# Performance work log

Measured on AMD Instinct MI355X. Metric: run time of the kernel, lower is better.

Reference implementation:

```python
import jax, jax.numpy as jnp
import numpy as np
import math

B, T, S, C, W = 32, 512, 128, 30, 10  # batch, seq, spans, candidates, max span width
D_CTX, D_ENT, H, V = 768, 300, 100, 200000
EPS = 1e-5
NEG = -1e30


def layer_norm(x, g, b):
    mu = jnp.mean(x, axis=-1, keepdims=True)
    var = jnp.mean((x - mu) ** 2, axis=-1, keepdims=True)
    return (x - mu) / jnp.sqrt(var + EPS) * g + b


def setup_inputs() -> dict:
    key = jax.random.key(0)
    ks = jax.random.split(key, 12)
    contextual_embeddings = jax.random.normal(ks[0], (B, T, D_CTX), jnp.float32)
    mask = jnp.ones((B, T), jnp.int32)
    starts = jax.random.randint(ks[1], (B, S), 0, T - W)
    widths = jax.random.randint(ks[2], (B, S), 0, W)
    ends = starts + widths  # inclusive end, AllenNLP convention
    # pad last 8 spans per example with -1 to exercise span masking
    pad = jnp.arange(S)[None, :] >= S - 8
    starts = jnp.where(pad, -1, starts)
    ends = jnp.where(pad, -1, ends)
    candidate_spans = jnp.stack([starts, ends], axis=-1)
    candidate_entities = jax.random.randint(ks[3], (B, S, C), 1, V)
    pri = jax.random.uniform(ks[4], (B, S, C), jnp.float32)
    candidate_entity_priors = pri / pri.sum(-1, keepdims=True)
    candidate_segment_ids = jnp.zeros((B, S, C), jnp.int32)
    # parameters
    entity_table = jax.random.normal(ks[5], (V, D_ENT), jnp.float32) * 0.02
    proj_W = jax.random.normal(ks[6], (D_ENT, D_CTX), jnp.float32) * 0.02
    proj_b = jnp.zeros((D_ENT,), jnp.float32)
    kg_g = jnp.ones((D_ENT,), jnp.float32)
    kg_b = jnp.zeros((D_ENT,), jnp.float32)
    ln_g = jnp.ones((D_ENT,), jnp.float32)
    ln_b = jnp.zeros((D_ENT,), jnp.float32)
    attn_W = jax.random.normal(ks[7], (1, D_ENT), jnp.float32) * 0.02
    attn_b = jnp.zeros((1,), jnp.float32)
    W1 = jax.random.normal(ks[8], (H, 2), jnp.float32) * 0.02
    b1 = jnp.zeros((H,), jnp.float32)
    W2 = jax.random.normal(ks[9], (1, H), jnp.float32) * 0.02
    b2 = jnp.zeros((1,), jnp.float32)
    return dict(contextual_embeddings=contextual_embeddings, mask=mask,
                candidate_spans=candidate_spans, candidate_entities=candidate_entities,
                candidate_entity_priors=candidate_entity_priors,
                candidate_segment_ids=candidate_segment_ids,
                entity_table=entity_table, proj_W=proj_W, proj_b=proj_b,
                kg_g=kg_g, kg_b=kg_b, ln_g=ln_g, ln_b=ln_b,
                attn_W=attn_W, attn_b=attn_b, W1=W1, b1=b1, W2=W2, b2=b2)


def reference(contextual_embeddings, mask, candidate_spans, candidate_entities,
              candidate_entity_priors, candidate_segment_ids, entity_table,
              proj_W, proj_b, kg_g, kg_b, ln_g, ln_b, attn_W, attn_b,
              W1, b1, W2, b2):
    # --- entity embedding lookup + KG layer norm ---
    ent_emb = layer_norm(entity_table[candidate_entities], kg_g, kg_b)  # (B,S,C,D)

    # --- bert -> kg projection ---
    proj = contextual_embeddings @ proj_W.T + proj_b  # (B,T,D_ENT)

    span_mask = candidate_spans[:, :, 0] > -1  # (B,S)

    # --- SelfAttentiveSpanExtractor ---
    att_logits = (proj @ attn_W.T + attn_b)[..., 0]  # (B,T)
    starts = candidate_spans[..., 0]
    ends = candidate_spans[..., 1]
    widths = ends - starts
    offs = jnp.arange(W)  # max span width
    idx = starts[..., None] + offs  # (B,S,W)
    valid = (offs <= widths[..., None]) & (idx >= 0) & (idx < T)
    idx_c = jnp.where(valid, idx, 0)
    idx_flat = idx_c.reshape(B, S * W)
    span_emb = jnp.take_along_axis(proj, idx_flat[..., None], axis=1).reshape(B, S, W, D_ENT)
    span_log = jnp.take_along_axis(att_logits, idx_flat, axis=1).reshape(B, S, W)
    attn = jax.nn.softmax(jnp.where(valid, span_log, NEG), axis=-1)  # (B,S,W)
    span_rep = jnp.einsum('bsw,bswd->bsd', attn, span_emb)
    span_rep = span_rep * span_mask[..., None].astype(span_rep.dtype)
    span_rep = layer_norm(span_rep, ln_g, ln_b)  # (B,S,D)

    # --- DotAttentionWithPrior ---
    scores = jnp.einsum('bsd,bscd->bsc', span_rep, ent_emb) / math.sqrt(D_ENT)
    feat = jnp.stack([scores, candidate_entity_priors], axis=-1)  # (B,S,C,2)
    h = jax.nn.relu(feat @ W1.T + b1)
    link = (h @ W2.T + b2)[..., 0]  # (B,S,C)
    entity_mask = candidate_entities > 0
    linking_scores = jnp.where(entity_mask, link, -10000.0)
    normed = jax.nn.softmax(linking_scores, axis=-1)
    weighted = jnp.einsum('bsc,bscd->bsd', normed, ent_emb)
    return linking_scores, weighted
```

## Files before the change

### kernel.cpp

```cpp
#include <hip/hip_runtime.h>
#include <hip/hip_bf16.h>
#include <math.h>

#define BB 32
#define TT 512
#define SS 128
#define CC 30
#define WW 10
#define DCTX 768
#define DENT 300
#define HH 100
#define EPSF 1e-5f
#define NEGF -1e30f

typedef __attribute__((ext_vector_type(8))) short bf16x8;
typedef __attribute__((ext_vector_type(4))) float f32x4;

#define NK  (DCTX / 32)
#define NCT 20

__device__ __forceinline__ float wave_sum(float v) {
    #pragma unroll
    for (int off = 32; off > 0; off >>= 1) v += __shfl_xor(v, off);
    return v;
}

__device__ __forceinline__ ushort f2bf(float f) {
    __hip_bfloat16 h = __float2bfloat16(f);
    return *reinterpret_cast<ushort*>(&h);
}

__device__ __forceinline__ float dot4(float4 a, float4 b) {
    return a.x*b.x + a.y*b.y + a.z*b.z + a.w*b.w;
}
__device__ __forceinline__ float hadd8(float4 a, float4 b) {
    return a.x+a.y+a.z+a.w + b.x+b.y+b.z+b.w;
}
__device__ __forceinline__ ushort4 cvt4(float4 v) {
    ushort4 h; h.x = f2bf(v.x); h.y = f2bf(v.y); h.z = f2bf(v.z); h.w = f2bf(v.w);
    return h;
}

__global__ __launch_bounds__(256) void wpre_kernel(
    const float* __restrict__ Wt, ushort* __restrict__ wpre)
{
    const int g = blockIdx.x * 256 + threadIdx.x;
    const int l = g & 63;
    const int t = (g >> 6) % NK;
    const int ct = g / (NK * 64);
    const int col = ct * 16 + (l & 15);
    const int k = t * 32 + (l >> 4) * 8;
    ushort4 h0 = {0, 0, 0, 0}, h1 = {0, 0, 0, 0};
    if (col < DENT) {
        float4 v0 = *(const float4*)(Wt + (size_t)col * DCTX + k);
        float4 v1 = *(const float4*)(Wt + (size_t)col * DCTX + k + 4);
        h0 = cvt4(v0); h1 = cvt4(v1);
    }
    *(ushort4*)(wpre + (size_t)g * 8)     = h0;
    *(ushort4*)(wpre + (size_t)g * 8 + 4) = h1;
}

#define GBM 64
#define LDA 40

__global__ __launch_bounds__(512) void gemm_proj_mfma(
    const float*  __restrict__ A,
    const ushort* __restrict__ wpre,
    const float*  __restrict__ bias,
    float* __restrict__ out)
{
    __shared__ ushort Al[2][GBM * LDA];
    const int tid = threadIdx.x;
    const int lane = tid & 63;
    const int wv = tid >> 6;
    const int wm = wv >> 2;
    const int wn = wv & 3;
    const int m0 = blockIdx.x * GBM;
    const int ar = tid >> 3;
    const int ak = (tid & 7) * 4;
    const int lr = lane & 15;
    const int kq = (lane >> 4) * 8;

    const float* aP = A + (size_t)(m0 + ar) * DCTX + ak;
    const ushort* bp = wpre + (size_t)wn * 5 * NK * 512 + (size_t)lane * 8;

    f32x4 acc[2][5];
    #pragma unroll
    for (int i = 0; i < 2; ++i)
        #pragma unroll
        for (int j = 0; j < 5; ++j)
            acc[i][j] = (f32x4){0.f, 0.f, 0.f, 0.f};

    bf16x8 cb[5], nb[5];
    #pragma unroll
    for (int j = 0; j < 5; ++j)
        cb[j] = *(const bf16x8*)(bp + (size_t)j * NK * 512);

#define STOREA(BUF, v_) (*(ushort4*)&Al[BUF][ar * LDA + ak] = cvt4(v_))

#define COMPUTE(BUF) do {                                                      \
        bf16x8 af_[2];                                                         \
        _Pragma("unroll")                                                      \
        for (int i_ = 0; i_ < 2; ++i_)                                         \
            af_[i_] = *(const bf16x8*)&Al[BUF][(wm*32 + i_*16 + lr)*LDA + kq]; \
        _Pragma("unroll")                                                      \
        for (int j_ = 0; j_ < 5; ++j_)                                         \
            acc[0][j_] = __builtin_amdgcn_mfma_f32_16x16x32_bf16(              \
                af_[0], cb[j_], acc[0][j_], 0, 0, 0);                          \
        _Pragma("unroll")                                                      \
        for (int j_ = 0; j_ < 5; ++j_)                                         \
            acc[1][j_] = __builtin_amdgcn_mfma_f32_16x16x32_bf16(              \
                af_[1], cb[j_], acc[1][j_], 0, 0, 0);                          \
    } while (0)

    float4 avA = *(const float4*)(aP);
    float4 avB = *(const float4*)(aP + 32);
    STOREA(0, avA);
    __syncthreads();

    #pragma unroll 1
    for (int kk = 0; kk < NK; kk += 2) {
        #pragma unroll
        for (int j = 0; j < 5; ++j)
            nb[j] = *(const bf16x8*)(bp + ((size_t)j * NK + kk + 1) * 512);
        if (kk + 2 < NK) avA = *(const float4*)(aP + (kk + 2) * 32);
        COMPUTE(0);
        STOREA(1, avB);
        __syncthreads();
        #pragma unroll
        for (int j = 0; j < 5; ++j) cb[j] = nb[j];
        if (kk + 2 < NK) {
            #pragma unroll
            for (int j = 0; j < 5; ++j)
                nb[j] = *(const bf16x8*)(bp + ((size_t)j * NK + kk + 2) * 512);
            avB = *(const float4*)(aP + (kk + 3) * 32);
        }
        COMPUTE(1);
        if (kk + 2 < NK) STOREA(0, avA);
        __syncthreads();
        #pragma unroll
        for (int j = 0; j < 5; ++j) cb[j] = nb[j];
    }

    const int lq = lane >> 4;
    #pragma unroll
    for (int j = 0; j < 5; ++j) {
        int col = wn * 80 + j * 16 + lr;
        if (col < DENT) {
            float bv = bias[col];
            #pragma unroll
            for (int i = 0; i < 2; ++i)
                #pragma unroll
                for (int r = 0; r < 4; ++r) {
                    int row = m0 + wm * 32 + i * 16 + lq * 4 + r;
                    out[(size_t)row * DENT + col] = acc[i][j][r] + bv;
                }
        }
    }
}

__global__ __launch_bounds__(256) void span_kernel(
    const float* __restrict__ proj,
    const int*   __restrict__ spans,
    const float* __restrict__ attn_W,
    const float* __restrict__ attn_b,
    const float* __restrict__ ln_g,
    const float* __restrict__ ln_b,
    const float* __restrict__ kg_g,
    const float* __restrict__ kg_b,
    float* __restrict__ srg_out,
    float* __restrict__ sgsb)
{
    const int bs = blockIdx.x * 4 + (threadIdx.x >> 6);
    const int b = bs >> 7;
    const int lane = threadIdx.x & 63;
    const int start = spans[bs * 2 + 0];
    const int end   = spans[bs * 2 + 1];
    const int width = end - start;
    const bool lo = lane < 11;
    const float4 z = make_float4(0.f, 0.f, 0.f, 0.f);

    const float4* attW4 = (const float4*)attn_W;
    float4 w0 = attW4[lane];
    float4 w1 = lo ? attW4[64 + lane] : z;

    float4 a0[WW], a1[WW];
    float slog[WW];
    bool vld[WW];
    #pragma unroll
    for (int w = 0; w < WW; ++w) {
        int idx = start + w;
        vld[w] = (w <= width) && (idx >= 0) && (idx < TT);
        const float4* pr = (const float4*)(proj + (size_t)(b * TT + (vld[w] ? idx : 0)) * DENT);
        a0[w] = pr[lane];
        a1[w] = lo ? pr[64 + lane] : z;
        slog[w] = dot4(a0[w], w0) + dot4(a1[w], w1);
    }
    const float ab = attn_b[0];
    #pragma unroll
    for (int w = 0; w < WW; ++w) {
        float r = wave_sum(slog[w]);
        slog[w] = vld[w] ? r + ab : NEGF;
    }
    float m = slog[0];
    #pragma unroll
    for (int w = 1; w < WW; ++w) m = fmaxf(m, slog[w]);
    float den = 0.f;
    float aw[WW];
    #pragma unroll
    for (int w = 0; w < WW; ++w) { aw[w] = expf(slog[w] - m); den += aw[w]; }
    const float inv = 1.f / den;
    const float msk = (start > -1) ? inv : 0.f;

    float4 acc0 = z, acc1 = z;
    #pragma unroll
    for (int w = 0; w < WW; ++w) {
        float c = aw[w] * msk;
        acc0.x = fmaf(c, a0[w].x, acc0.x); acc0.y = fmaf(c, a0[w].y, acc0.y);
        acc0.z = fmaf(c, a0[w].z, acc0.z); acc0.w = fmaf(c, a0[w].w, acc0.w);
        acc1.x = fmaf(c, a1[w].x, acc1.x); acc1.y = fmaf(c, a1[w].y, acc1.y);
        acc1.z = fmaf(c, a1[w].z, acc1.z); acc1.w = fmaf(c, a1[w].w, acc1.w);
    }
    float s1 = hadd8(acc0, acc1);
    float s2 = dot4(acc0, acc0) + dot4(acc1, acc1);
    #pragma unroll
    for (int off = 32; off > 0; off >>= 1) {
        s1 += __shfl_xor(s1, off);
        s2 += __shfl_xor(s2, off);
    }
    const float mu = s1 * (1.f / DENT);
    const float rstd = rsqrtf(s2 * (1.f / DENT) - mu * mu + EPSF);

    const float4* lg4 = (const float4*)ln_g;  const float4* lb4 = (const float4*)ln_b;
    const float4* gg4 = (const float4*)kg_g;  const float4* gb4 = (const float4*)kg_b;
    float pg = 0.f, pb = 0.f;
    float4* so = (float4*)(srg_out + (size_t)bs * DENT);
    {
        float4 g = lg4[lane], bb_ = lb4[lane], gg = gg4[lane], gb = gb4[lane];
        float4 val;
        val.x = fmaf((acc0.x - mu) * rstd, g.x, bb_.x);
        val.y = fmaf((acc0.y - mu) * rstd, g.y, bb_.y);
        val.z = fmaf((acc0.z - mu) * rstd, g.z, bb_.z);
        val.w = fmaf((acc0.w - mu) * rstd, g.w, bb_.w);
        float4 vg = make_float4(val.x * gg.x, val.y * gg.y, val.z * gg.z, val.w * gg.w);
        so[lane] = vg;
        pg += vg.x + vg.y + vg.z + vg.w;
        pb += val.x * gb.x + val.y * gb.y + val.z * gb.z + val.w * gb.w;
    }
    if (lo) {
        float4 g = lg4[64 + lane], bb_ = lb4[64 + lane], gg = gg4[64 + lane], gb = gb4[64 + lane];
        float4 val;
        val.x = fmaf((acc1.x - mu) * rstd, g.x, bb_.x);
        val.y = fmaf((acc1.y - mu) * rstd, g.y, bb_.y);
        val.z = fmaf((acc1.z - mu) * rstd, g.z, bb_.z);
        val.w = fmaf((acc1.w - mu) * rstd, g.w, bb_.w);
        float4 vg = make_float4(val.x * gg.x, val.y * gg.y, val.z * gg.z, val.w * gg.w);
        so[64 + lane] = vg;
        pg += vg.x + vg.y + vg.z + vg.w;
        pb += val.x * gb.x + val.y * gb.y + val.z * gb.z + val.w * gb.w;
    }
    #pragma unroll
    for (int off = 32; off > 0; off >>= 1) {
        pg += __shfl_xor(pg, off);
        pb += __shfl_xor(pb, off);
    }
    if (lane == 0) { sgsb[bs * 2 + 0] = pg; sgsb[bs * 2 + 1] = pb; }
}

__global__ __launch_bounds__(512) void final_fused(
    const float* __restrict__ srg,
    const float* __restrict__ sgsb,
    const int*   __restrict__ cand,
    const float* __restrict__ priors,
    const float* __restrict__ table,
    const float* __restrict__ W1,
    const float* __restrict__ b1,
    const float* __restrict__ W2,
    const float* __restrict__ b2,
    const float* __restrict__ kg_g,
    const float* __restrict__ kg_b,
    float* __restrict__ out_link,
    float* __restrict__ out_w)
{
    __shared__ float rows[CC][DENT];
    __shared__ float smu[CC], srs[CC], ssc[CC], sexp[CC];
    const int bs = blockIdx.x;
    const int tid = threadIdx.x;
    const int lane = tid & 63;
    const int wv = tid >> 6;
    const bool lo = lane < 11;
    const float4 z = make_float4(0.f, 0.f, 0.f, 0.f);

    const int c0 = wv, c1 = wv + 8, c2 = wv + 16, c3 = wv + 24;
    const bool has3 = (c3 < CC);
    const int e0 = cand[bs * CC + c0];
    const int e1 = cand[bs * CC + c1];
    const int e2 = cand[bs * CC + c2];
    const int e3 = has3 ? cand[bs * CC + c3] : e2;

    const float4* r0 = (const float4*)(table + (size_t)e0 * DENT);
    const float4* r1 = (const float4*)(table + (size_t)e1 * DENT);
    const float4* r2 = (const float4*)(table + (size_t)e2 * DENT);
    const float4* r3 = (const float4*)(table + (size_t)e3 * DENT);
    float4 xa0 = r0[lane], xa1 = r1[lane], xa2 = r2[lane], xa3 = r3[lane];
    float4 xb0 = lo ? r0[64 + lane] : z;
    float4 xb1 = lo ? r1[64 + lane] : z;
    float4 xb2 = lo ? r2[64 + lane] : z;
    float4 xb3 = lo ? r3[64 + lane] : z;

    const float4* sg4 = (const float4*)(srg + (size_t)bs * DENT);
    float4 g0 = sg4[lane];
    float4 g1 = lo ? sg4[64 + lane] : z;
    const float SG = sgsb[bs * 2 + 0];
    const float SB = sgsb[bs * 2 + 1];

    const float W1a0 = W1[2 * lane], W1b0 = W1[2 * lane + 1];
    const float B10 = b1[lane], W20 = W2[lane];
    float W1a1 = 0.f, W1b1 = 0.f, B11 = 0.f, W21 = 0.f;
    if (lane < HH - 64) {
        int j = lane + 64;
        W1a1 = W1[2 * j]; W1b1 = W1[2 * j + 1]; B11 = b1[j]; W21 = W2[j];
    }
    const float b2v = b2[0];
    const float p0 = priors[bs * CC + c0];
    const float p1 = priors[bs * CC + c1];
    const float p2 = priors[bs * CC + c2];
    const float p3 = has3 ? priors[bs * CC + c3] : 0.f;

    *(float4*)&rows[c0][lane * 4] = xa0;
    *(float4*)&rows[c1][lane * 4] = xa1;
    *(float4*)&rows[c2][lane * 4] = xa2;
    if (has3) *(float4*)&rows[c3][lane * 4] = xa3;
    if (lo) {
        *(float4*)&rows[c0][256 + lane * 4] = xb0;
        *(float4*)&rows[c1][256 + lane * 4] = xb1;
        *(float4*)&rows[c2][256 + lane * 4] = xb2;
        if (has3) *(float4*)&rows[c3][256 + lane * 4] = xb3;
    }

    float s1_0 = hadd8(xa0, xb0), s1_1 = hadd8(xa1, xb1);
    float s1_2 = hadd8(xa2, xb2), s1_3 = hadd8(xa3, xb3);
    float s2_0 = dot4(xa0, xa0) + dot4(xb0, xb0), s2_1 = dot4(xa1, xa1) + dot4(xb1, xb1);
    float s2_2 = dot4(xa2, xa2) + dot4(xb2, xb2), s2_3 = dot4(xa3, xa3) + dot4(xb3, xb3);
    float s3_0 = dot4(g0, xa0) + dot4(g1, xb0), s3_1 = dot4(g0, xa1) + dot4(g1, xb1);
    float s3_2 = dot4(g0, xa2) + dot4(g1, xb2), s3_3 = dot4(g0, xa3) + dot4(g1, xb3);
    #pragma unroll
    for (int off = 32; off > 0; off >>= 1) {
        s1_0 += __shfl_xor(s1_0, off); s1_1 += __shfl_xor(s1_1, off);
        s1_2 += __shfl_xor(s1_2, off); s1_3 += __shfl_xor(s1_3, off);
        s2_0 += __shfl_xor(s2_0, off); s2_1 += __shfl_xor(s2_1, off);
        s2_2 += __shfl_xor(s2_2, off); s2_3 += __shfl_xor(s2_3, off);
        s3_0 += __shfl_xor(s3_0, off); s3_1 += __shfl_xor(s3_1, off);
        s3_2 += __shfl_xor(s3_2, off); s3_3 += __shfl_xor(s3_3, off);
    }
    const float isd = rsqrtf((float)DENT);

#define CAND_TAIL(K, CK, EK, PK)                                               \
    do {                                                                       \
        float mu_ = s1_##K * (1.f / DENT);                                     \
        float rstd_ = rsqrtf(s2_##K * (1.f / DENT) - mu_ * mu_ + EPSF);        \
        float score_ = (rstd_ * (s3_##K - mu_ * SG) + SB) * isd;               \
        float h_ = fmaxf(fmaf(W1a0, score_, fmaf(W1b0, PK, B10)), 0.f);        \
        float h2_ = fmaxf(fmaf(W1a1, score_, fmaf(W1b1, PK, B11)), 0.f);       \
        float lp_ = fmaf(W21, h2_, W20 * h_);                                  \
        lp_ = wave_sum(lp_) + b2v;                                             \
        float link_ = (EK > 0) ? lp_ : -10000.0f;                              \
        if (lane == 0) {                                                       \
            smu[CK] = mu_; srs[CK] = rstd_; ssc[CK] = link_;                   \
            out_link[bs * CC + CK] = link_;                                    \
        }                                                                      \
    } while (0)

    CAND_TAIL(0, c0, e0, p0);
    CAND_TAIL(1, c1, e1, p1);
    CAND_TAIL(2, c2, e2, p2);
    if (has3) CAND_TAIL(3, c3, e3, p3);
    __syncthreads();

    if (tid < CC) {
        float m = ssc[0];
        #pragma unroll
        for (int c = 1; c < CC; ++c) m = fmaxf(m, ssc[c]);
        sexp[tid] = expf(ssc[tid] - m);
    }
    __syncthreads();

    const int d = tid;
    if (d < DENT) {
        float den = 0.f;
        #pragma unroll
        for (int c = 0; c < CC; ++c) den += sexp[c];
        const float inv = 1.f / den;
        float acc = 0.f, S2 = 0.f, sn = 0.f;
        #pragma unroll
        for (int c = 0; c < CC; ++c) {
            float n = sexp[c] * inv;
            float coef = n * srs[c];
            acc = fmaf(coef, rows[c][d], acc);
            S2 = fmaf(coef, smu[c], S2);
            sn += n;
        }
        out_w[(size_t)bs * DENT + d] = kg_g[d] * (acc - S2) + kg_b[d] * sn;
    }
}

extern "C" void kernel_launch(void* const* d_in, const int* in_sizes, int n_in,
                              void* d_out, int out_size, void* d_ws, size_t ws_size,
                              hipStream_t stream) {
    const float* ctx    = (const float*)d_in[0];
    const int*   spans  = (const int*)d_in[2];
    const int*   cand   = (const int*)d_in[3];
    const float* priors = (const float*)d_in[4];
    const float* table  = (const float*)d_in[6];
    const float* projW  = (const float*)d_in[7];
    const float* projb  = (const float*)d_in[8];
    const float* kg_g   = (const float*)d_in[9];
    const float* kg_b   = (const float*)d_in[10];
    const float* ln_g   = (const float*)d_in[11];
    const float* ln_b   = (const float*)d_in[12];
    const float* attW   = (const float*)d_in[13];
    const float* attb   = (const float*)d_in[14];
    const float* W1     = (const float*)d_in[15];
    const float* b1     = (const float*)d_in[16];
    const float* W2     = (const float*)d_in[17];
    const float* b2     = (const float*)d_in[18];

    float* proj = (float*)d_ws;
    float* srg  = proj + (size_t)BB * TT * DENT;
    float* sgsb = srg + (size_t)BB * SS * DENT;
    ushort* wpre = (ushort*)srg;

    float* out_link = (float*)d_out;
    float* out_w    = out_link + (size_t)BB * SS * CC;

    wpre_kernel<<<NCT * NK * 64 / 256, 256, 0, stream>>>(projW, wpre);
    gemm_proj_mfma<<<BB * TT / GBM, 512, 0, stream>>>(ctx, wpre, projb, proj);
    span_kernel<<<BB * SS / 4, 256, 0, stream>>>(proj, spans, attW, attb,
                                                 ln_g, ln_b, kg_g, kg_b, srg, sgsb);
    final_fused<<<BB * SS, 512, 0, stream>>>(srg, sgsb, cand, priors, table,
                                             W1, b1, W2, b2, kg_g, kg_b,
                                             out_link, out_w);
}
```

Before: 95.21 us.

## Store projection as bf16 and fuse span pooling into final kernel

The projection GEMM now writes its output as bf16 with a padded row stride of 320 instead of fp32. The separate span kernel is removed, and its attention pooling, layer norm and kg-gain preparation run in wave 0 of the final fused kernel, with results passed through shared memory. This removes one launch, the srg/sgsb round trip through global memory, and halves projection traffic. In exchange it adds bf16 rounding on proj and places the span work serially on one wave before the other waves can compute scores.

```diff
diff --git a/kernel.cpp b/kernel.cpp
--- a/kernel.cpp
+++ b/kernel.cpp
@@ -12,6 +12,7 @@
 #define HH 100
 #define EPSF 1e-5f
 #define NEGF -1e30f
+#define PSTR 320
 
 typedef __attribute__((ext_vector_type(8))) short bf16x8;
 typedef __attribute__((ext_vector_type(4))) float f32x4;
@@ -28,6 +29,16 @@
 __device__ __forceinline__ ushort f2bf(float f) {
     __hip_bfloat16 h = __float2bfloat16(f);
     return *reinterpret_cast<ushort*>(&h);
+}
+
+__device__ __forceinline__ float bf2f1(short s) {
+    union { unsigned u; float f; } t;
+    t.u = ((unsigned)(unsigned short)s) << 16;
+    return t.f;
+}
+__device__ __forceinline__ void bf8_cvt(bf16x8 v, float4& lo, float4& hi) {
+    lo.x = bf2f1(v[0]); lo.y = bf2f1(v[1]); lo.z = bf2f1(v[2]); lo.w = bf2f1(v[3]);
+    hi.x = bf2f1(v[4]); hi.y = bf2f1(v[5]); hi.z = bf2f1(v[6]); hi.w = bf2f1(v[7]);
 }
 
 __device__ __forceinline__ float dot4(float4 a, float4 b) {
@@ -52,9 +63,8 @@
     const int k = t * 32 + (l >> 4) * 8;
     ushort4 h0 = {0, 0, 0, 0}, h1 = {0, 0, 0, 0};
     if (col < DENT) {
-        float4 v0 = *(const float4*)(Wt + (size_t)col * DCTX + k);
-        float4 v1 = *(const float4*)(Wt + (size_t)col * DCTX + k + 4);
-        h0 = cvt4(v0); h1 = cvt4(v1);
+        h0 = cvt4(*(const float4*)(Wt + (size_t)col * DCTX + k));
+        h1 = cvt4(*(const float4*)(Wt + (size_t)col * DCTX + k + 4));
     }
     *(ushort4*)(wpre + (size_t)g * 8)     = h0;
     *(ushort4*)(wpre + (size_t)g * 8 + 4) = h1;
@@ -67,7 +77,7 @@
     const float*  __restrict__ A,
     const ushort* __restrict__ wpre,
     const float*  __restrict__ bias,
-    float* __restrict__ out)
+    ushort* __restrict__ out)
 {
     __shared__ ushort Al[2][GBM * LDA];
     const int tid = threadIdx.x;
@@ -146,145 +156,42 @@
     #pragma unroll
     for (int j = 0; j < 5; ++j) {
         int col = wn * 80 + j * 16 + lr;
-        if (col < DENT) {
-            float bv = bias[col];
+        float bv = (col < DENT) ? bias[col] : 0.f;
+        #pragma unroll
+        for (int i = 0; i < 2; ++i)
             #pragma unroll
-            for (int i = 0; i < 2; ++i)
-                #pragma unroll
-                for (int r = 0; r < 4; ++r) {
-                    int row = m0 + wm * 32 + i * 16 + lq * 4 + r;
-                    out[(size_t)row * DENT + col] = acc[i][j][r] + bv;
-                }
-        }
-    }
-}
-
-__global__ __launch_bounds__(256) void span_kernel(
-    const float* __restrict__ proj,
-    const int*   __restrict__ spans,
-    const float* __restrict__ attn_W,
-    const float* __restrict__ attn_b,
-    const float* __restrict__ ln_g,
-    const float* __restrict__ ln_b,
-    const float* __restrict__ kg_g,
-    const float* __restrict__ kg_b,
-    float* __restrict__ srg_out,
-    float* __restrict__ sgsb)
-{
-    const int bs = blockIdx.x * 4 + (threadIdx.x >> 6);
-    const int b = bs >> 7;
-    const int lane = threadIdx.x & 63;
-    const int start = spans[bs * 2 + 0];
-    const int end   = spans[bs * 2 + 1];
-    const int width = end - start;
-    const bool lo = lane < 11;
-    const float4 z = make_float4(0.f, 0.f, 0.f, 0.f);
-
-    const float4* attW4 = (const float4*)attn_W;
-    float4 w0 = attW4[lane];
-    float4 w1 = lo ? attW4[64 + lane] : z;
-
-    float4 a0[WW], a1[WW];
-    float slog[WW];
-    bool vld[WW];
-    #pragma unroll
-    for (int w = 0; w < WW; ++w) {
-        int idx = start + w;
-        vld[w] = (w <= width) && (idx >= 0) && (idx < TT);
-        const float4* pr = (const float4*)(proj + (size_t)(b * TT + (vld[w] ? idx : 0)) * DENT);
-        a0[w] = pr[lane];
-        a1[w] = lo ? pr[64 + lane] : z;
-        slog[w] = dot4(a0[w], w0) + dot4(a1[w], w1);
-    }
-    const float ab = attn_b[0];
-    #pragma unroll
-    for (int w = 0; w < WW; ++w) {
-        float r = wave_sum(slog[w]);
-        slog[w] = vld[w] ? r + ab : NEGF;
-    }
-    float m = slog[0];
-    #pragma unroll
-    for (int w = 1; w < WW; ++w) m = fmaxf(m, slog[w]);
-    float den = 0.f;
-    float aw[WW];
-    #pragma unroll
-    for (int w = 0; w < WW; ++w) { aw[w] = expf(slog[w] - m); den += aw[w]; }
-    const float inv = 1.f / den;
-    const float msk = (start > -1) ? inv : 0.f;
-
-    float4 acc0 = z, acc1 = z;
-    #pragma unroll
-    for (int w = 0; w < WW; ++w) {
-        float c = aw[w] * msk;
-        acc0.x = fmaf(c, a0[w].x, acc0.x); acc0.y = fmaf(c, a0[w].y, acc0.y);
-        acc0.z = fmaf(c, a0[w].z, acc0.z); acc0.w = fmaf(c, a0[w].w, acc0.w);
-        acc1.x = fmaf(c, a1[w].x, acc1.x); acc1.y = fmaf(c, a1[w].y, acc1.y);
-        acc1.z = fmaf(c, a1[w].z, acc1.z); acc1.w = fmaf(c, a1[w].w, acc1.w);
-    }
-    float s1 = hadd8(acc0, acc1);
-    float s2 = dot4(acc0, acc0) + dot4(acc1, acc1);
-    #pragma unroll
-    for (int off = 32; off > 0; off >>= 1) {
-        s1 += __shfl_xor(s1, off);
-        s2 += __shfl_xor(s2, off);
-    }
-    const float mu = s1 * (1.f / DENT);
-    const float rstd = rsqrtf(s2 * (1.f / DENT) - mu * mu + EPSF);
-
-    const float4* lg4 = (const float4*)ln_g;  const float4* lb4 = (const float4*)ln_b;
-    const float4* gg4 = (const float4*)kg_g;  const float4* gb4 = (const float4*)kg_b;
-    float pg = 0.f, pb = 0.f;
-    float4* so = (float4*)(srg_out + (size_t)bs * DENT);
-    {
-        float4 g = lg4[lane], bb_ = lb4[lane], gg = gg4[lane], gb = gb4[lane];
-        float4 val;
-        val.x = fmaf((acc0.x - mu) * rstd, g.x, bb_.x);
-        val.y = fmaf((acc0.y - mu) * rstd, g.y, bb_.y);
-        val.z = fmaf((acc0.z - mu) * rstd, g.z, bb_.z);
-        val.w = fmaf((acc0.w - mu) * rstd, g.w, bb_.w);
-        float4 vg = make_float4(val.x * gg.x, val.y * gg.y, val.z * gg.z, val.w * gg.w);
-        so[lane] = vg;
-        pg += vg.x + vg.y + vg.z + vg.w;
-        pb += val.x * gb.x + val.y * gb.y + val.z * gb.z + val.w * gb.w;
-    }
-    if (lo) {
-        float4 g = lg4[64 + lane], bb_ = lb4[64 + lane], gg = gg4[64 + lane], gb = gb4[64 + lane];
-        float4 val;
-        val.x = fmaf((acc1.x - mu) * rstd, g.x, bb_.x);
-        val.y = fmaf((acc1.y - mu) * rstd, g.y, bb_.y);
-        val.z = fmaf((acc1.z - mu) * rstd, g.z, bb_.z);
-        val.w = fmaf((acc1.w - mu) * rstd, g.w, bb_.w);
-        float4 vg = make_float4(val.x * gg.x, val.y * gg.y, val.z * gg.z, val.w * gg.w);
-        so[64 + lane] = vg;
-        pg += vg.x + vg.y + vg.z + vg.w;
-        pb += val.x * gb.x + val.y * gb.y + val.z * gb.z + val.w * gb.w;
-    }
-    #pragma unroll
-    for (int off = 32; off > 0; off >>= 1) {
-        pg += __shfl_xor(pg, off);
-        pb += __shfl_xor(pb, off);
-    }
-    if (lane == 0) { sgsb[bs * 2 + 0] = pg; sgsb[bs * 2 + 1] = pb; }
+            for (int r = 0; r < 4; ++r) {
+                int row = m0 + wm * 32 + i * 16 + lq * 4 + r;
+                out[(size_t)row * PSTR + col] = f2bf(acc[i][j][r] + bv);
+            }
+    }
 }
 
 __global__ __launch_bounds__(512) void final_fused(
-    const float* __restrict__ srg,
-    const float* __restrict__ sgsb,
-    const int*   __restrict__ cand,
-    const float* __restrict__ priors,
-    const float* __restrict__ table,
-    const float* __restrict__ W1,
-    const float* __restrict__ b1,
-    const float* __restrict__ W2,
-    const float* __restrict__ b2,
-    const float* __restrict__ kg_g,
-    const float* __restrict__ kg_b,
+    const ushort* __restrict__ proj,
+    const int*    __restrict__ spans,
+    const float*  __restrict__ attW,
+    const float*  __restrict__ attb,
+    const float*  __restrict__ ln_g,
+    const float*  __restrict__ ln_b,
+    const float*  __restrict__ kg_g,
+    const float*  __restrict__ kg_b,
+    const int*    __restrict__ cand,
+    const float*  __restrict__ priors,
+    const float*  __restrict__ table,
+    const float*  __restrict__ W1,
+    const float*  __restrict__ b1,
+    const float*  __restrict__ W2,
+    const float*  __restrict__ b2,
     float* __restrict__ out_link,
     float* __restrict__ out_w)
 {
     __shared__ float rows[CC][DENT];
+    __shared__ float s_srg[PSTR];
     __shared__ float smu[CC], srs[CC], ssc[CC], sexp[CC];
+    __shared__ float sSG, sSB;
     const int bs = blockIdx.x;
+    const int b = bs >> 7;
     const int tid = threadIdx.x;
     const int lane = tid & 63;
     const int wv = tid >> 6;
@@ -308,25 +215,6 @@
     float4 xb2 = lo ? r2[64 + lane] : z;
     float4 xb3 = lo ? r3[64 + lane] : z;
 
-    const float4* sg4 = (const float4*)(srg + (size_t)bs * DENT);
-    float4 g0 = sg4[lane];
-    float4 g1 = lo ? sg4[64 + lane] : z;
-    const float SG = sgsb[bs * 2 + 0];
-    const float SB = sgsb[bs * 2 + 1];
-
-    const float W1a0 = W1[2 * lane], W1b0 = W1[2 * lane + 1];
-    const float B10 = b1[lane], W20 = W2[lane];
-    float W1a1 = 0.f, W1b1 = 0.f, B11 = 0.f, W21 = 0.f;
-    if (lane < HH - 64) {
-        int j = lane + 64;
-        W1a1 = W1[2 * j]; W1b1 = W1[2 * j + 1]; B11 = b1[j]; W21 = W2[j];
-    }
-    const float b2v = b2[0];
-    const float p0 = priors[bs * CC + c0];
-    const float p1 = priors[bs * CC + c1];
-    const float p2 = priors[bs * CC + c2];
-    const float p3 = has3 ? priors[bs * CC + c3] : 0.f;
-
     *(float4*)&rows[c0][lane * 4] = xa0;
     *(float4*)&rows[c1][lane * 4] = xa1;
     *(float4*)&rows[c2][lane * 4] = xa2;
@@ -342,17 +230,136 @@
     float s1_2 = hadd8(xa2, xb2), s1_3 = hadd8(xa3, xb3);
     float s2_0 = dot4(xa0, xa0) + dot4(xb0, xb0), s2_1 = dot4(xa1, xa1) + dot4(xb1, xb1);
     float s2_2 = dot4(xa2, xa2) + dot4(xb2, xb2), s2_3 = dot4(xa3, xa3) + dot4(xb3, xb3);
-    float s3_0 = dot4(g0, xa0) + dot4(g1, xb0), s3_1 = dot4(g0, xa1) + dot4(g1, xb1);
-    float s3_2 = dot4(g0, xa2) + dot4(g1, xb2), s3_3 = dot4(g0, xa3) + dot4(g1, xb3);
     #pragma unroll
     for (int off = 32; off > 0; off >>= 1) {
         s1_0 += __shfl_xor(s1_0, off); s1_1 += __shfl_xor(s1_1, off);
         s1_2 += __shfl_xor(s1_2, off); s1_3 += __shfl_xor(s1_3, off);
         s2_0 += __shfl_xor(s2_0, off); s2_1 += __shfl_xor(s2_1, off);
         s2_2 += __shfl_xor(s2_2, off); s2_3 += __shfl_xor(s2_3, off);
+    }
+
+    if (wv == 0) {
+        const int start = spans[bs * 2 + 0];
+        const int end   = spans[bs * 2 + 1];
+        const int width = end - start;
+        const bool L   = lane < 40;
+        const int  dl  = (L ? lane : 39) * 8;
+        const bool ga  = L && (dl < DENT);
+        const bool gb4 = L && (dl + 4 < DENT);
+
+        float4 w0v = ga  ? *(const float4*)(attW + dl)     : z;
+        float4 w1v = gb4 ? *(const float4*)(attW + dl + 4) : z;
+
+        float slog[WW];
+        int rbase[WW];
+        bool vld[WW];
+        #pragma unroll
+        for (int w = 0; w < WW; ++w) {
+            int idx = start + w;
+            vld[w] = (w <= width) && (idx >= 0) && (idx < TT);
+            rbase[w] = (b * TT + (vld[w] ? idx : 0)) * PSTR;
+            bf16x8 v = *(const bf16x8*)(proj + rbase[w] + dl);
+            float4 plo, phi; bf8_cvt(v, plo, phi);
+            if (!L) { plo = z; phi = z; }
+            slog[w] = dot4(plo, w0v) + dot4(phi, w1v);
+        }
+        const float ab = attb[0];
+        #pragma unroll
+        for (int w = 0; w < WW; ++w) {
+            float r = wave_sum(slog[w]);
+            slog[w] = vld[w] ? r + ab : NEGF;
+        }
+        float m = slog[0];
+        #pragma unroll
+        for (int w = 1; w < WW; ++w) m = fmaxf(m, slog[w]);
+        float den = 0.f;
+        float aw[WW];
+        #pragma unroll
+        for (int w = 0; w < WW; ++w) { aw[w] = expf(slog[w] - m); den += aw[w]; }
+        const float msk = (start > -1) ? (1.f / den) : 0.f;
+
+        float4 acc0 = z, acc1 = z;
+        #pragma unroll
+        for (int w = 0; w < WW; ++w) {
+            bf16x8 v = *(const bf16x8*)(proj + rbase[w] + dl);
+            float4 plo, phi; bf8_cvt(v, plo, phi);
+            if (!L) { plo = z; phi = z; }
+            float c = aw[w] * msk;
+            acc0.x = fmaf(c, plo.x, acc0.x); acc0.y = fmaf(c, plo.y, acc0.y);
+            acc0.z = fmaf(c, plo.z, acc0.z); acc0.w = fmaf(c, plo.w, acc0.w);
+            acc1.x = fmaf(c, phi.x, acc1.x); acc1.y = fmaf(c, phi.y, acc1.y);
+            acc1.z = fmaf(c, phi.z, acc1.z); acc1.w = fmaf(c, phi.w, acc1.w);
+        }
+        float s1 = hadd8(acc0, acc1);
+        float s2 = dot4(acc0, acc0) + dot4(acc1, acc1);
+        #pragma unroll
+        for (int off = 32; off > 0; off >>= 1) {
+            s1 += __shfl_xor(s1, off);
+            s2 += __shfl_xor(s2, off);
+        }
+        const float mu = s1 * (1.f / DENT);
+        const float rstd = rsqrtf(s2 * (1.f / DENT) - mu * mu + EPSF);
+
+        float4 lg0 = ga  ? *(const float4*)(ln_g + dl)     : z;
+        float4 lg1 = gb4 ? *(const float4*)(ln_g + dl + 4) : z;
+        float4 lb0 = ga  ? *(const float4*)(ln_b + dl)     : z;
+        float4 lb1 = gb4 ? *(const float4*)(ln_b + dl + 4) : z;
+        float4 gg0 = ga  ? *(const float4*)(kg_g + dl)     : z;
+        float4 gg1 = gb4 ? *(const float4*)(kg_g + dl + 4) : z;
+        float4 gbv0 = ga  ? *(const float4*)(kg_b + dl)     : z;
+        float4 gbv1 = gb4 ? *(const float4*)(kg_b + dl + 4) : z;
+
+        float4 val0, val1, vg0, vg1;
+        val0.x = fmaf((acc0.x - mu) * rstd, lg0.x, lb0.x);
+        val0.y = fmaf((acc0.y - mu) * rstd, lg0.y, lb0.y);
+        val0.z = fmaf((acc0.z - mu) * rstd, lg0.z, lb0.z);
+        val0.w = fmaf((acc0.w - mu) * rstd, lg0.w, lb0.w);
+        val1.x = fmaf((acc1.x - mu) * rstd, lg1.x, lb1.x);
+        val1.y = fmaf((acc1.y - mu) * rstd, lg1.y, lb1.y);
+        val1.z = fmaf((acc1.z - mu) * rstd, lg1.z, lb1.z);
+        val1.w = fmaf((acc1.w - mu) * rstd, lg1.w, lb1.w);
+        vg0 = make_float4(val0.x*gg0.x, val0.y*gg0.y, val0.z*gg0.z, val0.w*gg0.w);
+        vg1 = make_float4(val1.x*gg1.x, val1.y*gg1.y, val1.z*gg1.z, val1.w*gg1.w);
+        if (L) {
+            *(float4*)&s_srg[dl]     = vg0;
+            *(float4*)&s_srg[dl + 4] = vg1;
+        }
+        float pg = hadd8(vg0, vg1);
+        float pb = dot4(val0, gbv0) + dot4(val1, gbv1);
+        #pragma unroll
+        for (int off = 32; off > 0; off >>= 1) {
+            pg += __shfl_xor(pg, off);
+            pb += __shfl_xor(pb, off);
+        }
+        if (lane == 0) { sSG = pg; sSB = pb; }
+    }
+    __syncthreads();
+
+    const float4 g0 = *(const float4*)&s_srg[lane * 4];
+    const float4 g1 = lo ? *(const float4*)&s_srg[256 + lane * 4] : z;
+    const float SG = sSG;
+    const float SB = sSB;
+
+    float s3_0 = dot4(g0, xa0) + dot4(g1, xb0), s3_1 = dot4(g0, xa1) + dot4(g1, xb1);
+    float s3_2 = dot4(g0, xa2) + dot4(g1, xb2), s3_3 = dot4(g0, xa3) + dot4(g1, xb3);
+    #pragma unroll
+    for (int off = 32; off > 0; off >>= 1) {
         s3_0 += __shfl_xor(s3_0, off); s3_1 += __shfl_xor(s3_1, off);
         s3_2 += __shfl_xor(s3_2, off); s3_3 += __shfl_xor(s3_3, off);
     }
+
+    const float W1a0 = W1[2 * lane], W1b0 = W1[2 * lane + 1];
+    const float B10 = b1[lane], W20 = W2[lane];
+    float W1a1 = 0.f, W1b1 = 0.f, B11 = 0.f, W21 = 0.f;
+    if (lane < HH - 64) {
+        int j = lane + 64;
+        W1a1 = W1[2 * j]; W1b1 = W1[2 * j + 1]; B11 = b1[j]; W21 = W2[j];
+    }
+    const float b2v = b2[0];
+    const float p0 = priors[bs * CC + c0];
+    const float p1 = priors[bs * CC + c1];
+    const float p2 = priors[bs * CC + c2];
+    const float p3 = has3 ? priors[bs * CC + c3] : 0.f;
     const float isd = rsqrtf((float)DENT);
 
 #define CAND_TAIL(K, CK, EK, PK)                                               \
@@ -425,19 +432,17 @@
     const float* W2     = (const float*)d_in[17];
     const float* b2     = (const float*)d_in[18];
 
-    float* proj = (float*)d_ws;
-    float* srg  = proj + (size_t)BB * TT * DENT;
-    float* sgsb = srg + (size_t)BB * SS * DENT;
-    ushort* wpre = (ushort*)srg;
+    ushort* proj = (ushort*)d_ws;
+    ushort* wpre = proj + (size_t)BB * TT * PSTR;
 
     float* out_link = (float*)d_out;
     float* out_w    = out_link + (size_t)BB * SS * CC;
 
     wpre_kernel<<<NCT * NK * 64 / 256, 256, 0, stream>>>(projW, wpre);
     gemm_proj_mfma<<<BB * TT / GBM, 512, 0, stream>>>(ctx, wpre, projb, proj);
-    span_kernel<<<BB * SS / 4, 256, 0, stream>>>(proj, spans, attW, attb,
-                                                 ln_g, ln_b, kg_g, kg_b, srg, sgsb);
-    final_fused<<<BB * SS, 512, 0, stream>>>(srg, sgsb, cand, priors, table,
-                                             W1, b1, W2, b2, kg_g, kg_b,
+    final_fused<<<BB * SS, 512, 0, stream>>>(proj, spans, attW, attb,
+                                             ln_g, ln_b, kg_g, kg_b,
+                                             cand, priors, table,
+                                             W1, b1, W2, b2,
                                              out_link, out_w);
 }
```

New measurement: 212.3 us. 2.23x slower.

## Process two span rows per block in final kernel with early gathers

Applied to the files above, without the earlier changes.

The final fused kernel now handles two (batch, span) pairs per block, issuing the entity-table gathers for both up front so the second pair's loads overlap the first pair's reductions and softmax. The grid is halved. This aims to hide gather latency and amortise block overhead, at the cost of many more live registers (up to 16 extra float4 per thread), which may reduce occupancy, plus an extra barrier.

```diff
diff --git a/kernel.cpp b/kernel.cpp
--- a/kernel.cpp
+++ b/kernel.cpp
@@ -52,9 +52,8 @@
     const int k = t * 32 + (l >> 4) * 8;
     ushort4 h0 = {0, 0, 0, 0}, h1 = {0, 0, 0, 0};
     if (col < DENT) {
-        float4 v0 = *(const float4*)(Wt + (size_t)col * DCTX + k);
-        float4 v1 = *(const float4*)(Wt + (size_t)col * DCTX + k + 4);
-        h0 = cvt4(v0); h1 = cvt4(v1);
+        h0 = cvt4(*(const float4*)(Wt + (size_t)col * DCTX + k));
+        h1 = cvt4(*(const float4*)(Wt + (size_t)col * DCTX + k + 4));
     }
     *(ushort4*)(wpre + (size_t)g * 8)     = h0;
     *(ushort4*)(wpre + (size_t)g * 8 + 4) = h1;
@@ -283,8 +282,10 @@
     float* __restrict__ out_w)
 {
     __shared__ float rows[CC][DENT];
-    __shared__ float smu[CC], srs[CC], ssc[CC], sexp[CC];
-    const int bs = blockIdx.x;
+    __shared__ float smuA[CC], srsA[CC], sscA[CC], sexpA[CC];
+    __shared__ float smuB[CC], srsB[CC], sscB[CC], sexpB[CC];
+    const int bs0 = blockIdx.x * 2;
+    const int bs1 = bs0 + 1;
     const int tid = threadIdx.x;
     const int lane = tid & 63;
     const int wv = tid >> 6;
@@ -293,26 +294,40 @@
 
     const int c0 = wv, c1 = wv + 8, c2 = wv + 16, c3 = wv + 24;
     const bool has3 = (c3 < CC);
-    const int e0 = cand[bs * CC + c0];
-    const int e1 = cand[bs * CC + c1];
-    const int e2 = cand[bs * CC + c2];
-    const int e3 = has3 ? cand[bs * CC + c3] : e2;
-
-    const float4* r0 = (const float4*)(table + (size_t)e0 * DENT);
-    const float4* r1 = (const float4*)(table + (size_t)e1 * DENT);
-    const float4* r2 = (const float4*)(table + (size_t)e2 * DENT);
-    const float4* r3 = (const float4*)(table + (size_t)e3 * DENT);
-    float4 xa0 = r0[lane], xa1 = r1[lane], xa2 = r2[lane], xa3 = r3[lane];
-    float4 xb0 = lo ? r0[64 + lane] : z;
-    float4 xb1 = lo ? r1[64 + lane] : z;
-    float4 xb2 = lo ? r2[64 + lane] : z;
-    float4 xb3 = lo ? r3[64 + lane] : z;
-
-    const float4* sg4 = (const float4*)(srg + (size_t)bs * DENT);
-    float4 g0 = sg4[lane];
-    float4 g1 = lo ? sg4[64 + lane] : z;
-    const float SG = sgsb[bs * 2 + 0];
-    const float SB = sgsb[bs * 2 + 1];
+
+    const int e00 = cand[bs0 * CC + c0];
+    const int e01 = cand[bs0 * CC + c1];
+    const int e02 = cand[bs0 * CC + c2];
+    const int e03 = has3 ? cand[bs0 * CC + c3] : e02;
+    const float4* r00 = (const float4*)(table + (size_t)e00 * DENT);
+    const float4* r01 = (const float4*)(table + (size_t)e01 * DENT);
+    const float4* r02 = (const float4*)(table + (size_t)e02 * DENT);
+    const float4* r03 = (const float4*)(table + (size_t)e03 * DENT);
+    float4 p0 = r00[lane], p1 = r01[lane], p2 = r02[lane], p3 = r03[lane];
+    float4 q0 = lo ? r00[64 + lane] : z;
+    float4 q1 = lo ? r01[64 + lane] : z;
+    float4 q2 = lo ? r02[64 + lane] : z;
+    float4 q3 = lo ? r03[64 + lane] : z;
+
+    const int e10 = cand[bs1 * CC + c0];
+    const int e11 = cand[bs1 * CC + c1];
+    const int e12 = cand[bs1 * CC + c2];
+    const int e13 = has3 ? cand[bs1 * CC + c3] : e12;
+    const float4* r10 = (const float4*)(table + (size_t)e10 * DENT);
+    const float4* r11 = (const float4*)(table + (size_t)e11 * DENT);
+    const float4* r12 = (const float4*)(table + (size_t)e12 * DENT);
+    const float4* r13 = (const float4*)(table + (size_t)e13 * DENT);
+    float4 u0 = r10[lane], u1 = r11[lane], u2 = r12[lane], u3 = r13[lane];
+    float4 v0 = lo ? r10[64 + lane] : z;
+    float4 v1 = lo ? r11[64 + lane] : z;
+    float4 v2 = lo ? r12[64 + lane] : z;
+    float4 v3 = lo ? r13[64 + lane] : z;
+
+    const float4* sg0 = (const float4*)(srg + (size_t)bs0 * DENT);
+    float4 g00 = sg0[lane];
+    float4 g01 = lo ? sg0[64 + lane] : z;
+    const float SG0 = sgsb[bs0 * 2 + 0];
+    const float SB0 = sgsb[bs0 * 2 + 1];
 
     const float W1a0 = W1[2 * lane], W1b0 = W1[2 * lane + 1];
     const float B10 = b1[lane], W20 = W2[lane];
@@ -322,85 +337,158 @@
         W1a1 = W1[2 * j]; W1b1 = W1[2 * j + 1]; B11 = b1[j]; W21 = W2[j];
     }
     const float b2v = b2[0];
-    const float p0 = priors[bs * CC + c0];
-    const float p1 = priors[bs * CC + c1];
-    const float p2 = priors[bs * CC + c2];
-    const float p3 = has3 ? priors[bs * CC + c3] : 0.f;
-
-    *(float4*)&rows[c0][lane * 4] = xa0;
-    *(float4*)&rows[c1][lane * 4] = xa1;
-    *(float4*)&rows[c2][lane * 4] = xa2;
-    if (has3) *(float4*)&rows[c3][lane * 4] = xa3;
-    if (lo) {
-        *(float4*)&rows[c0][256 + lane * 4] = xb0;
-        *(float4*)&rows[c1][256 + lane * 4] = xb1;
-        *(float4*)&rows[c2][256 + lane * 4] = xb2;
-        if (has3) *(float4*)&rows[c3][256 + lane * 4] = xb3;
-    }
-
-    float s1_0 = hadd8(xa0, xb0), s1_1 = hadd8(xa1, xb1);
-    float s1_2 = hadd8(xa2, xb2), s1_3 = hadd8(xa3, xb3);
-    float s2_0 = dot4(xa0, xa0) + dot4(xb0, xb0), s2_1 = dot4(xa1, xa1) + dot4(xb1, xb1);
-    float s2_2 = dot4(xa2, xa2) + dot4(xb2, xb2), s2_3 = dot4(xa3, xa3) + dot4(xb3, xb3);
-    float s3_0 = dot4(g0, xa0) + dot4(g1, xb0), s3_1 = dot4(g0, xa1) + dot4(g1, xb1);
-    float s3_2 = dot4(g0, xa2) + dot4(g1, xb2), s3_3 = dot4(g0, xa3) + dot4(g1, xb3);
-    #pragma unroll
-    for (int off = 32; off > 0; off >>= 1) {
-        s1_0 += __shfl_xor(s1_0, off); s1_1 += __shfl_xor(s1_1, off);
-        s1_2 += __shfl_xor(s1_2, off); s1_3 += __shfl_xor(s1_3, off);
-        s2_0 += __shfl_xor(s2_0, off); s2_1 += __shfl_xor(s2_1, off);
-        s2_2 += __shfl_xor(s2_2, off); s2_3 += __shfl_xor(s2_3, off);
-        s3_0 += __shfl_xor(s3_0, off); s3_1 += __shfl_xor(s3_1, off);
-        s3_2 += __shfl_xor(s3_2, off); s3_3 += __shfl_xor(s3_3, off);
-    }
     const float isd = rsqrtf((float)DENT);
 
-#define CAND_TAIL(K, CK, EK, PK)                                               \
+#define CAND_TAIL(SMU, SRS, SSC, OUTBS, S1, S2, S3, CK, EK, PK, SG_, SB_)      \
     do {                                                                       \
-        float mu_ = s1_##K * (1.f / DENT);                                     \
-        float rstd_ = rsqrtf(s2_##K * (1.f / DENT) - mu_ * mu_ + EPSF);        \
-        float score_ = (rstd_ * (s3_##K - mu_ * SG) + SB) * isd;               \
+        float mu_ = S1 * (1.f / DENT);                                         \
+        float rstd_ = rsqrtf(S2 * (1.f / DENT) - mu_ * mu_ + EPSF);            \
+        float score_ = (rstd_ * (S3 - mu_ * SG_) + SB_) * isd;                 \
         float h_ = fmaxf(fmaf(W1a0, score_, fmaf(W1b0, PK, B10)), 0.f);        \
         float h2_ = fmaxf(fmaf(W1a1, score_, fmaf(W1b1, PK, B11)), 0.f);       \
         float lp_ = fmaf(W21, h2_, W20 * h_);                                  \
         lp_ = wave_sum(lp_) + b2v;                                             \
         float link_ = (EK > 0) ? lp_ : -10000.0f;                              \
         if (lane == 0) {                                                       \
-            smu[CK] = mu_; srs[CK] = rstd_; ssc[CK] = link_;                   \
-            out_link[bs * CC + CK] = link_;                                    \
+            SMU[CK] = mu_; SRS[CK] = rstd_; SSC[CK] = link_;                   \
+            out_link[(OUTBS) * CC + CK] = link_;                               \
         }                                                                      \
     } while (0)
 
-    CAND_TAIL(0, c0, e0, p0);
-    CAND_TAIL(1, c1, e1, p1);
-    CAND_TAIL(2, c2, e2, p2);
-    if (has3) CAND_TAIL(3, c3, e3, p3);
+    {
+        *(float4*)&rows[c0][lane * 4] = p0;
+        *(float4*)&rows[c1][lane * 4] = p1;
+        *(float4*)&rows[c2][lane * 4] = p2;
+        if (has3) *(float4*)&rows[c3][lane * 4] = p3;
+        if (lo) {
+            *(float4*)&rows[c0][256 + lane * 4] = q0;
+            *(float4*)&rows[c1][256 + lane * 4] = q1;
+            *(float4*)&rows[c2][256 + lane * 4] = q2;
+            if (has3) *(float4*)&rows[c3][256 + lane * 4] = q3;
+        }
+        float s1_0 = hadd8(p0, q0), s1_1 = hadd8(p1, q1);
+        float s1_2 = hadd8(p2, q2), s1_3 = hadd8(p3, q3);
+        float s2_0 = dot4(p0, p0) + dot4(q0, q0), s2_1 = dot4(p1, p1) + dot4(q1, q1);
+        float s2_2 = dot4(p2, p2) + dot4(q2, q2), s2_3 = dot4(p3, p3) + dot4(q3, q3);
+        float s3_0 = dot4(g00, p0) + dot4(g01, q0), s3_1 = dot4(g00, p1) + dot4(g01, q1);
+        float s3_2 = dot4(g00, p2) + dot4(g01, q2), s3_3 = dot4(g00, p3) + dot4(g01, q3);
+        #pragma unroll
+        for (int off = 32; off > 0; off >>= 1) {
+            s1_0 += __shfl_xor(s1_0, off); s1_1 += __shfl_xor(s1_1, off);
+            s1_2 += __shfl_xor(s1_2, off); s1_3 += __shfl_xor(s1_3, off);
+            s2_0 += __shfl_xor(s2_0, off); s2_1 += __shfl_xor(s2_1, off);
+            s2_2 += __shfl_xor(s2_2, off); s2_3 += __shfl_xor(s2_3, off);
+            s3_0 += __shfl_xor(s3_0, off); s3_1 += __shfl_xor(s3_1, off);
+            s3_2 += __shfl_xor(s3_2, off); s3_3 += __shfl_xor(s3_3, off);
+        }
+        const float pr0 = priors[bs0 * CC + c0];
+        const float pr1 = priors[bs0 * CC + c1];
+        const float pr2 = priors[bs0 * CC + c2];
+        const float pr3 = has3 ? priors[bs0 * CC + c3] : 0.f;
+        CAND_TAIL(smuA, srsA, sscA, bs0, s1_0, s2_0, s3_0, c0, e00, pr0, SG0, SB0);
+        CAND_TAIL(smuA, srsA, sscA, bs0, s1_1, s2_1, s3_1, c1, e01, pr1, SG0, SB0);
+        CAND_TAIL(smuA, srsA, sscA, bs0, s1_2, s2_2, s3_2, c2, e02, pr2, SG0, SB0);
+        if (has3)
+            CAND_TAIL(smuA, srsA, sscA, bs0, s1_3, s2_3, s3_3, c3, e03, pr3, SG0, SB0);
+    }
     __syncthreads();
 
     if (tid < CC) {
-        float m = ssc[0];
-        #pragma unroll
-        for (int c = 1; c < CC; ++c) m = fmaxf(m, ssc[c]);
-        sexp[tid] = expf(ssc[tid] - m);
+        float m = sscA[0];
+        #pragma unroll
+        for (int c = 1; c < CC; ++c) m = fmaxf(m, sscA[c]);
+        sexpA[tid] = expf(sscA[tid] - m);
     }
     __syncthreads();
 
-    const int d = tid;
-    if (d < DENT) {
-        float den = 0.f;
-        #pragma unroll
-        for (int c = 0; c < CC; ++c) den += sexp[c];
-        const float inv = 1.f / den;
-        float acc = 0.f, S2 = 0.f, sn = 0.f;
-        #pragma unroll
-        for (int c = 0; c < CC; ++c) {
-            float n = sexp[c] * inv;
-            float coef = n * srs[c];
-            acc = fmaf(coef, rows[c][d], acc);
-            S2 = fmaf(coef, smu[c], S2);
-            sn += n;
-        }
-        out_w[(size_t)bs * DENT + d] = kg_g[d] * (acc - S2) + kg_b[d] * sn;
+    {
+        const float4* sg1 = (const float4*)(srg + (size_t)bs1 * DENT);
+        float4 g10 = sg1[lane];
+        float4 g11 = lo ? sg1[64 + lane] : z;
+        const float SG1 = sgsb[bs1 * 2 + 0];
+        const float SB1 = sgsb[bs1 * 2 + 1];
+        float s1_0 = hadd8(u0, v0), s1_1 = hadd8(u1, v1);
+        float s1_2 = hadd8(u2, v2), s1_3 = hadd8(u3, v3);
+        float s2_0 = dot4(u0, u0) + dot4(v0, v0), s2_1 = dot4(u1, u1) + dot4(v1, v1);
+        float s2_2 = dot4(u2, u2) + dot4(v2, v2), s2_3 = dot4(u3, u3) + dot4(v3, v3);
+        float s3_0 = dot4(g10, u0) + dot4(g11, v0), s3_1 = dot4(g10, u1) + dot4(g11, v1);
+        float s3_2 = dot4(g10, u2) + dot4(g11, v2), s3_3 = dot4(g10, u3) + dot4(g11, v3);
+        #pragma unroll
+        for (int off = 32; off > 0; off >>= 1) {
+            s1_0 += __shfl_xor(s1_0, off); s1_1 += __shfl_xor(s1_1, off);
+            s1_2 += __shfl_xor(s1_2, off); s1_3 += __shfl_xor(s1_3, off);
+            s2_0 += __shfl_xor(s2_0, off); s2_1 += __shfl_xor(s2_1, off);
+            s2_2 += __shfl_xor(s2_2, off); s2_3 += __shfl_xor(s2_3, off);
+            s3_0 += __shfl_xor(s3_0, off); s3_1 += __shfl_xor(s3_1, off);
+            s3_2 += __shfl_xor(s3_2, off); s3_3 += __shfl_xor(s3_3, off);
+        }
+        const float pr0 = priors[bs1 * CC + c0];
+        const float pr1 = priors[bs1 * CC + c1];
+        const float pr2 = priors[bs1 * CC + c2];
+        const float pr3 = has3 ? priors[bs1 * CC + c3] : 0.f;
+        CAND_TAIL(smuB, srsB, sscB, bs1, s1_0, s2_0, s3_0, c0, e10, pr0, SG1, SB1);
+        CAND_TAIL(smuB, srsB, sscB, bs1, s1_1, s2_1, s3_1, c1, e11, pr1, SG1, SB1);
+        CAND_TAIL(smuB, srsB, sscB, bs1, s1_2, s2_2, s3_2, c2, e12, pr2, SG1, SB1);
+        if (has3)
+            CAND_TAIL(smuB, srsB, sscB, bs1, s1_3, s2_3, s3_3, c3, e13, pr3, SG1, SB1);
+    }
+    {
+        const int d = tid;
+        if (d < DENT) {
+            float den = 0.f;
+            #pragma unroll
+            for (int c = 0; c < CC; ++c) den += sexpA[c];
+            const float inv = 1.f / den;
+            float acc = 0.f, S2 = 0.f, sn = 0.f;
+            #pragma unroll
+            for (int c = 0; c < CC; ++c) {
+                float n = sexpA[c] * inv;
+                float coef = n * srsA[c];
+                acc = fmaf(coef, rows[c][d], acc);
+                S2 = fmaf(coef, smuA[c], S2);
+                sn += n;
+            }
+            out_w[(size_t)bs0 * DENT + d] = kg_g[d] * (acc - S2) + kg_b[d] * sn;
+        }
+    }
+    __syncthreads();
+
+    *(float4*)&rows[c0][lane * 4] = u0;
+    *(float4*)&rows[c1][lane * 4] = u1;
+    *(float4*)&rows[c2][lane * 4] = u2;
+    if (has3) *(float4*)&rows[c3][lane * 4] = u3;
+    if (lo) {
+        *(float4*)&rows[c0][256 + lane * 4] = v0;
+        *(float4*)&rows[c1][256 + lane * 4] = v1;
+        *(float4*)&rows[c2][256 + lane * 4] = v2;
+        if (has3) *(float4*)&rows[c3][256 + lane * 4] = v3;
+    }
+    if (tid < CC) {
+        float m = sscB[0];
+        #pragma unroll
+        for (int c = 1; c < CC; ++c) m = fmaxf(m, sscB[c]);
+        sexpB[tid] = expf(sscB[tid] - m);
+    }
+    __syncthreads();
+
+    {
+        const int d = tid;
+        if (d < DENT) {
+            float den = 0.f;
+            #pragma unroll
+            for (int c = 0; c < CC; ++c) den += sexpB[c];
+            const float inv = 1.f / den;
+            float acc = 0.f, S2 = 0.f, sn = 0.f;
+            #pragma unroll
+            for (int c = 0; c < CC; ++c) {
+                float n = sexpB[c] * inv;
+                float coef = n * srsB[c];
+                acc = fmaf(coef, rows[c][d], acc);
+                S2 = fmaf(coef, smuB[c], S2);
+                sn += n;
+            }
+            out_w[(size_t)bs1 * DENT + d] = kg_g[d] * (acc - S2) + kg_b[d] * sn;
+        }
     }
 }
 
@@ -437,7 +525,7 @@
     gemm_proj_mfma<<<BB * TT / GBM, 512, 0, stream>>>(ctx, wpre, projb, proj);
     span_kernel<<<BB * SS / 4, 256, 0, stream>>>(proj, spans, attW, attb,
                                                  ln_g, ln_b, kg_g, kg_b, srg, sgsb);
-    final_fused<<<BB * SS, 512, 0, stream>>>(srg, sgsb, cand, priors, table,
-                                             W1, b1, W2, b2, kg_g, kg_b,
-                                             out_link, out_w);
-}
+    final_fused<<<BB * SS / 2, 512, 0, stream>>>(srg, sgsb, cand, priors, table,
+                                                 W1, b1, W2, b2, kg_g, kg_b,
+                                                 out_link, out_w);
+}
```

Measured after the change: 138.5 us. 1.45x slower.
